# Performance work log

Hardware: AMD Instinct MI355X
Metric: run time of the kernel (lower is better)

Reference implementation:

```python
import jax, jax.numpy as jnp
import numpy as np
from jax.scipy.linalg import cho_solve

N, D, T, K, P = 4000, 256, 52, 20, 100
EPS = 1e-8


def _make_kernel(length_scale):
    # RBF kernel over time grid with the same jitter-doubling rule as the torch code.
    t = np.arange(T, dtype=np.float32)
    sq = (t[None, :] - t[:, None]) ** 2
    Kmat = np.exp(-0.5 * sq / np.float32(length_scale) ** 2).astype(np.float32)
    jitter = 1e-4
    eye = np.eye(T, dtype=np.float32)
    while True:
        if np.linalg.cond(Kmat + jitter * eye) < 1e4:
            break
        jitter *= 2
        if jitter > 0.1:
            break
    return jnp.asarray(Kmat + jitter * eye)

K_LAMBDA = _make_kernel(T / 4)  # lambda GP kernel, shared across all k
K_PHI = _make_kernel(T / 3)     # phi GP kernel, shared across all k


def setup_inputs() -> dict:
    key = jax.random.key(0)
    ks = jax.random.split(key, 7)
    lambda_ = jax.random.normal(ks[0], (N, K, T), dtype=jnp.float32)
    phi = jax.random.normal(ks[1], (K, D, T), dtype=jnp.float32)
    gamma = 0.1 * jax.random.normal(ks[2], (P, K), dtype=jnp.float32)
    G = jax.random.normal(ks[3], (N, P), dtype=jnp.float32)
    Y = (jax.random.uniform(ks[4], (N, D, T)) < 0.05).astype(jnp.float32)
    logit_prev_t = jax.random.normal(ks[5], (D, T), dtype=jnp.float32) - 3.0
    event_times = jax.random.randint(ks[6], (N, D), 0, T)
    return dict(lambda_=lambda_, phi=phi, gamma=gamma, G=G, Y=Y,
                logit_prev_t=logit_prev_t, event_times=event_times)


def reference(lambda_, phi, gamma, G, Y, logit_prev_t, event_times):
    # --- forward: softmax over topics, sigmoid disease probs, mixture ---
    theta = jax.nn.softmax(lambda_, axis=1)          # [N,K,T]
    phi_prob = jax.nn.sigmoid(phi)                   # [K,D,T]
    pi = jnp.einsum('nkt,kdt->ndt', theta, phi_prob) # [N,D,T]
    pi = jnp.clip(pi, EPS, 1.0 - EPS)

    # --- survival data loss ---
    tgrid = jnp.arange(T)[None, None, :]             # [1,1,T]
    e = event_times[:, :, None]                      # [N,D,1]
    mask_before = (tgrid < e).astype(pi.dtype)
    mask_at = (tgrid == e).astype(pi.dtype)
    log_pi = jnp.log(pi)
    log_1mpi = jnp.log1p(-pi)
    loss_censored = -jnp.sum(log_1mpi * mask_before)
    loss_event = -jnp.sum(log_pi * mask_at * Y)
    loss_no_event = -jnp.sum(log_1mpi * mask_at * (1.0 - Y))
    data_loss = (loss_censored + loss_event + loss_no_event) / N

    # --- GP prior loss: batched cholesky solves replace per-sample loops ---
    L_lam = jnp.linalg.cholesky(K_LAMBDA)            # [T,T]
    L_phi = jnp.linalg.cholesky(K_PHI)               # [T,T]
    mean_lam = G @ gamma                             # [N,K]
    dev_lam = (lambda_ - mean_lam[:, :, None]).reshape(N * K, T)  # [N*K,T]
    v_lam = cho_solve((L_lam, True), dev_lam.T)      # [T,N*K]
    gp_lambda = 0.5 * jnp.sum(dev_lam.T * v_lam)
    dev_phi = (phi - logit_prev_t[None, :, :]).reshape(K * D, T)  # [K*D,T]
    v_phi = cho_solve((L_phi, True), dev_phi.T)      # [T,K*D]
    gp_phi = 0.5 * jnp.sum(dev_phi.T * v_phi)
    gp_loss = gp_lambda / N + gp_phi / D

    return data_loss + gp_loss
```

## Files before the change

kernel.cpp:

```cpp
#include <hip/hip_runtime.h>
#include <math.h>
#include <string.h>

#define Nn 4000
#define Dd 256
#define Tt 52
#define Kk 20
#define Pp 100
#define CH 4
#define TC 13
#define GRID_D ((Nn / 8) * CH)

#define OFF_W       0
#define OFF_MLAM_P  5408
#define OFF_MPHI_P  343408
#define OFF_DLP     397488
#define OFF_EVP     399488
#define OFF_PHIP    655488
#define OFF_THETA   921728

#define GR_ROWS 128

#define RB_PHIP0   0
#define RB_THETA0  52
#define RB_GPHI0   865
#define RB_GLAM0   885
#define RB_EVY0    1010
#define RB_TOTAL   2010

__global__ __launch_bounds__(256) void prep_kernel(
    const float* __restrict__ lam, const float* __restrict__ phi,
    const float* __restrict__ gamma, const float* __restrict__ G,
    const float* __restrict__ logit_prev, const int* __restrict__ ev,
    const float* __restrict__ Y,
    float* __restrict__ theta_t, float* __restrict__ phip_t,
    unsigned int* __restrict__ evy,
    float* __restrict__ Mlam_p, float* __restrict__ Mphi_p) {
    __shared__ float rows[GR_ROWS][56];
    __shared__ float meanv[GR_ROWS];
    const int bx = blockIdx.x, tid = threadIdx.x;

    if (bx < RB_THETA0) {
        int gid = bx * 256 + tid;
        int d = gid / Tt, t = gid - d * Tt;
        float v[Kk];
#pragma unroll
        for (int k = 0; k < Kk; ++k) {
            float x = phi[k * (Dd * Tt) + gid];
            v[k] = 1.f / (1.f + __expf(-x));
        }
#pragma unroll
        for (int k = 0; k < Kk; ++k)
            phip_t[((size_t)t * Kk + k) * Dd + d] = v[k];
        return;
    }
    if (bx < RB_GPHI0) {
        int gid = (bx - RB_THETA0) * 256 + tid;
        if (gid >= Nn * Tt) return;
        int n = gid / Tt, t = gid - n * Tt;
        const float* base = lam + n * Kk * Tt + t;
        float v[Kk];
        float m = -1e30f;
#pragma unroll
        for (int k = 0; k < Kk; ++k) { v[k] = base[k * Tt]; m = fmaxf(m, v[k]); }
        float s = 0.f;
#pragma unroll
        for (int k = 0; k < Kk; ++k) { v[k] = __expf(v[k] - m); s += v[k]; }
        float inv = 1.f / s;
        float* o = theta_t + ((size_t)t * Nn + n) * Kk;
#pragma unroll
        for (int k = 0; k < Kk; ++k) o[k] = v[k] * inv;
        return;
    }
    if (bx < RB_GLAM0) {
        int slot = bx - RB_GPHI0;
        int ta = tid % 13, tb = tid / 13;
        float acc[4][4] = {};
        for (int it = 0; it < 2; ++it) {
            int R0 = (slot * 2 + it) * GR_ROWS;
            __syncthreads();
            for (int idx = tid; idx < GR_ROWS * Tt; idx += 256) {
                int r = idx / Tt, t = idx - r * Tt;
                int R = R0 + r;
                rows[r][t] = phi[R * Tt + t] - logit_prev[(R & 255) * Tt + t];
            }
            __syncthreads();
            if (tb < 13) {
                for (int r = 0; r < GR_ROWS; ++r) {
                    float4 a = *(const float4*)&rows[r][4 * ta];
                    float4 b = *(const float4*)&rows[r][4 * tb];
                    float av[4] = {a.x, a.y, a.z, a.w};
                    float bv[4] = {b.x, b.y, b.z, b.w};
#pragma unroll
                    for (int i = 0; i < 4; ++i)
#pragma unroll
                        for (int j = 0; j < 4; ++j) acc[i][j] += av[i] * bv[j];
                }
            }
        }
        if (tb < 13)
#pragma unroll
            for (int i = 0; i < 4; ++i)
#pragma unroll
                for (int j = 0; j < 4; ++j)
                    Mphi_p[slot * 2704 + (4 * ta + i) * Tt + 4 * tb + j] = acc[i][j];
        return;
    }
    if (bx < RB_EVY0) {
        int slot = bx - RB_GLAM0;
        int ta = tid % 13, tb = tid / 13;
        float acc[4][4] = {};
        for (int it = 0; it < 5; ++it) {
            int R0 = (slot * 5 + it) * GR_ROWS;
            __syncthreads();
            if (tid < GR_ROWS) {
                int R = R0 + tid;
                int n = R / Kk, k = R - n * Kk;
                float m = 0.f;
                for (int p = 0; p < Pp; ++p) m += G[n * Pp + p] * gamma[p * Kk + k];
                meanv[tid] = m;
            }
            __syncthreads();
            for (int idx = tid; idx < GR_ROWS * Tt; idx += 256) {
                int r = idx / Tt, t = idx - r * Tt;
                int R = R0 + r;
                rows[r][t] = lam[R * Tt + t] - meanv[r];
            }
            __syncthreads();
            if (tb < 13) {
                for (int r = 0; r < GR_ROWS; ++r) {
                    float4 a = *(const float4*)&rows[r][4 * ta];
                    float4 b = *(const float4*)&rows[r][4 * tb];
                    float av[4] = {a.x, a.y, a.z, a.w};
                    float bv[4] = {b.x, b.y, b.z, b.w};
#pragma unroll
                    for (int i = 0; i < 4; ++i)
#pragma unroll
                        for (int j = 0; j < 4; ++j) acc[i][j] += av[i] * bv[j];
                }
            }
        }
        if (tb < 13)
#pragma unroll
            for (int i = 0; i < 4; ++i)
#pragma unroll
                for (int j = 0; j < 4; ++j)
                    Mlam_p[slot * 2704 + (4 * ta + i) * Tt + 4 * tb + j] = acc[i][j];
        return;
    }
    {
        int idx = bx - RB_EVY0;
        int ng = idx >> 1, half = idx & 1;
        int n0 = ng * 8 + half * 4;
        unsigned a = 0;
#pragma unroll
        for (int g = 0; g < 4; ++g) {
            int nd = (n0 + g) * Dd + tid;
            unsigned e = (unsigned)ev[nd] & 63u;
            float y = __builtin_nontemporal_load(Y + (size_t)nd * Tt + e);
            a |= (e | (y > 0.5f ? 128u : 0u)) << (8 * g);
        }
        evy[((size_t)ng * Dd + tid) * 2 + half] = a;
        return;
    }
}

__global__ __launch_bounds__(256) void data_kernel(const float* __restrict__ theta_t,
                                                   const float* __restrict__ phip_t,
                                                   const uint2* __restrict__ evy,
                                                   float* __restrict__ DLp) {
    __shared__ float wsum[4];
    const int tid = threadIdx.x;
    const int d = tid;
    const int ng = blockIdx.x >> 2;
    const int t0 = (blockIdx.x & 3) * TC;
    const int n0 = ng * 8;

    uint2 ee = evy[(size_t)ng * Dd + d];
    int e[8];
    float Yv[8], acc[8], pie[8], prod[8];
#pragma unroll
    for (int g = 0; g < 8; ++g) {
        unsigned byte = ((g < 4 ? ee.x : ee.y) >> (8 * (g & 3))) & 255u;
        e[g] = (int)(byte & 63u);
        Yv[g] = (byte & 128u) ? 1.f : 0.f;
        acc[g] = 0.f; prod[g] = 1.f; pie[g] = 0.5f;
    }

    for (int j = 0; j < TC; ++j) {
        int t = t0 + j;
        float pv[Kk];
        const float* pt = phip_t + (size_t)t * (Kk * Dd) + d;
#pragma unroll
        for (int k = 0; k < Kk; ++k) pv[k] = pt[k * Dd];
#pragma unroll
        for (int g = 0; g < 8; ++g) {
            const float4* th = (const float4*)(theta_t + ((size_t)t * Nn + n0 + g) * Kk);
            float4 a0 = th[0], a1 = th[1], a2 = th[2], a3 = th[3], a4 = th[4];
            float pi = a0.x * pv[0] + a0.y * pv[1] + a0.z * pv[2] + a0.w * pv[3]
                     + a1.x * pv[4] + a1.y * pv[5] + a1.z * pv[6] + a1.w * pv[7]
                     + a2.x * pv[8] + a2.y * pv[9] + a2.z * pv[10] + a2.w * pv[11]
                     + a3.x * pv[12] + a3.y * pv[13] + a3.z * pv[14] + a3.w * pv[15]
                     + a4.x * pv[16] + a4.y * pv[17] + a4.z * pv[18] + a4.w * pv[19];
            pi = fminf(fmaxf(pi, 1e-8f), 1.0f - 1e-8f);
            prod[g] *= (t <= e[g]) ? (1.f - pi) : 1.f;
            pie[g] = (t == e[g]) ? pi : pie[g];
        }
        if ((j & 3) == 3 || j == TC - 1) {
#pragma unroll
            for (int g = 0; g < 8; ++g) { acc[g] += __logf(prod[g]); prod[g] = 1.f; }
        }
    }
    float tsum = 0.f;
#pragma unroll
    for (int g = 0; g < 8; ++g)
        tsum += acc[g] + Yv[g] * (__logf(pie[g]) - __logf(1.f - pie[g]));
    for (int off = 32; off; off >>= 1) tsum += __shfl_down(tsum, off, 64);
    if ((tid & 63) == 0) wsum[tid >> 6] = tsum;
    __syncthreads();
    if (tid == 0)
        DLp[blockIdx.x] = -(wsum[0] + wsum[1] + wsum[2] + wsum[3]);
}

__global__ __launch_bounds__(1024) void final_kernel(const float* __restrict__ ws,
                                                     float* __restrict__ out) {
    const int tid = threadIdx.x;
    double s = 0.0;
    for (int i = tid; i < 2704; i += 1024) {
        double ml = 0.0, mp = 0.0;
        for (int b = 0; b < 125; ++b) ml += (double)ws[OFF_MLAM_P + b * 2704 + i];
        for (int b = 0; b < 20; ++b)  mp += (double)ws[OFF_MPHI_P + b * 2704 + i];
        s += (double)ws[OFF_W + i] * ml + (double)ws[OFF_W + 2704 + i] * mp;
    }
    double dl = 0.0;
    for (int i = tid; i < GRID_D; i += 1024) dl += (double)ws[OFF_DLP + i];
    s += dl / Nn;
    __shared__ double red[1024];
    red[tid] = s;
    __syncthreads();
    for (int off = 512; off; off >>= 1) {
        if (tid < off) red[tid] += red[tid + off];
        __syncthreads();
    }
    if (tid == 0) out[0] = (float)red[0];
}


static void build_K_f(double ls_in, float Kf[52][52]) {
    float ls = (float)ls_in;
    float ls2 = ls * ls;
    for (int i = 0; i < 52; ++i)
        for (int j = 0; j < 52; ++j) {
            float sq = (float)((i - j) * (i - j));
            float arg = (-0.5f * sq) / ls2;
            Kf[i][j] = expf(arg);
        }
}

static void jacobi_eig(double a[52][52], double ev[52]) {
    const int n = 52;
    for (int sweep = 0; sweep < 100; ++sweep) {
        double off = 0;
        for (int p = 0; p < n - 1; ++p)
            for (int q = p + 1; q < n; ++q) off += a[p][q] * a[p][q];
        if (off < 1e-24) break;
        for (int p = 0; p < n - 1; ++p)
            for (int q = p + 1; q < n; ++q) {
                double apq = a[p][q];
                if (fabs(apq) < 1e-300) continue;
                double th = (a[q][q] - a[p][p]) / (2.0 * apq);
                double t = (th >= 0 ? 1.0 : -1.0) / (fabs(th) + sqrt(th * th + 1.0));
                double c = 1.0 / sqrt(t * t + 1.0), s = t * c;
                for (int i = 0; i < n; ++i) {
                    double aip = a[i][p], aiq = a[i][q];
                    a[i][p] = c * aip - s * aiq;
                    a[i][q] = s * aip + c * aiq;
                }
                for (int i = 0; i < n; ++i) {
                    double api = a[p][i], aqi = a[q][i];
                    a[p][i] = c * api - s * aqi;
                    a[q][i] = s * api + c * aqi;
                }
            }
    }
    for (int i = 0; i < n; ++i) ev[i] = a[i][i];
}

static void build_A(const float Kf[52][52], double jitter, double A[52][52]) {
    float jf = (float)jitter;
    for (int i = 0; i < 52; ++i)
        for (int j = 0; j < 52; ++j) A[i][j] = (double)Kf[i][j];
    for (int i = 0; i < 52; ++i) A[i][i] = (double)(float)(Kf[i][i] + jf);
}

static double cond_of(const float Kf[52][52], double jitter) {
    double A[52][52], ev[52];
    build_A(Kf, jitter, A);
    jacobi_eig(A, ev);
    double mx = 0.0, mn = 1e300;
    for (int i = 0; i < 52; ++i) {
        double a = fabs(ev[i]);
        if (a > mx) mx = a;
        if (a < mn) mn = a;
    }
    if (mn <= 0.0) return 1e300;
    return mx / mn;
}

static double find_jitter(const float Kf[52][52]) {
    double jitter = 1e-4;
    while (true) {
        if (cond_of(Kf, jitter) < 1e4) break;
        jitter *= 2.0;
        if (jitter > 0.1) break;
    }
    return jitter;
}

static void chol_inv_scaled(const float Kf[52][52], double jitter, double scale,
                            float* out) {
    const int n = 52;
    double A[52][52], L[52][52];
    build_A(Kf, jitter, A);
    memset(L, 0, sizeof(L));
    for (int j = 0; j < n; ++j) {
        double s = A[j][j];
        for (int k = 0; k < j; ++k) s -= L[j][k] * L[j][k];
        L[j][j] = sqrt(s);
        for (int i = j + 1; i < n; ++i) {
            double v = A[i][j];
            for (int k = 0; k < j; ++k) v -= L[i][k] * L[j][k];
            L[i][j] = v / L[j][j];
        }
    }
    for (int c = 0; c < n; ++c) {
        double y[52], x[52];
        for (int i = 0; i < n; ++i) {
            double v = (i == c) ? 1.0 : 0.0;
            for (int k = 0; k < i; ++k) v -= L[i][k] * y[k];
            y[i] = v / L[i][i];
        }
        for (int i = n - 1; i >= 0; --i) {
            double v = y[i];
            for (int k = i + 1; k < n; ++k) v -= L[k][i] * x[k];
            x[i] = v / L[i][i];
        }
        for (int i = 0; i < n; ++i) out[i * 52 + c] = (float)(x[i] * scale);
    }
}

struct KinvInit {
    float* w;
    KinvInit() {
        if (hipHostMalloc((void**)&w, 5408 * sizeof(float)) != hipSuccess)
            w = (float*)malloc(5408 * sizeof(float));
        float Kf[52][52];
        build_K_f(52.0 / 4.0, Kf);
        chol_inv_scaled(Kf, find_jitter(Kf), 0.5 / Nn, w);
        build_K_f(52.0 / 3.0, Kf);
        chol_inv_scaled(Kf, find_jitter(Kf), 0.5 / Dd, w + 2704);
    }
};
static KinvInit g_kinv;


extern "C" void kernel_launch(void* const* d_in, const int* in_sizes, int n_in,
                              void* d_out, int out_size, void* d_ws, size_t ws_size,
                              hipStream_t stream) {
    (void)in_sizes; (void)n_in; (void)out_size; (void)ws_size;
    const float* lam        = (const float*)d_in[0];
    const float* phi        = (const float*)d_in[1];
    const float* gamma      = (const float*)d_in[2];
    const float* G          = (const float*)d_in[3];
    const float* Y          = (const float*)d_in[4];
    const float* logit_prev = (const float*)d_in[5];
    const int*   ev         = (const int*)d_in[6];
    float* out = (float*)d_out;
    float* ws  = (float*)d_ws;

    hipMemcpyAsync(ws + OFF_W, g_kinv.w, 5408 * sizeof(float),
                   hipMemcpyHostToDevice, stream);

    prep_kernel<<<RB_TOTAL, 256, 0, stream>>>(
        lam, phi, gamma, G, logit_prev, ev, Y,
        ws + OFF_THETA, ws + OFF_PHIP, (unsigned int*)(ws + OFF_EVP),
        ws + OFF_MLAM_P, ws + OFF_MPHI_P);
    data_kernel<<<GRID_D, 256, 0, stream>>>(
        ws + OFF_THETA, ws + OFF_PHIP, (const uint2*)(ws + OFF_EVP),
        ws + OFF_DLP);
    final_kernel<<<1, 1024, 0, stream>>>(ws, out);
}
```

Baseline: 442.8 us.

## Fuse final reduction into data kernel and reduce Gram partials in-block

The Gram-matrix blocks in the prep kernel now dot their partial 52x52 accumulators with the inverse-kernel weights and block-reduce to a single scalar, replacing the large partial-matrix writes. The final kernel is removed: the last data_kernel block, detected through an atomic counter, sums the partial scalars and data-loss partials. The data kernel also stages the theta tile into shared memory once per block rather than each thread reading it from global memory. This saves a launch and the slow single-block final reduction, at the cost of extra syncs and a threadfence/atomic handshake.

```diff
diff --git a/kernel.cpp b/kernel.cpp
--- a/kernel.cpp
+++ b/kernel.cpp
@@ -12,12 +12,12 @@
 #define GRID_D ((Nn / 8) * CH)
 
 #define OFF_W       0
-#define OFF_MLAM_P  5408
-#define OFF_MPHI_P  343408
-#define OFF_DLP     397488
-#define OFF_EVP     399488
-#define OFF_PHIP    655488
-#define OFF_THETA   921728
+#define OFF_GPART   5408
+#define OFF_DLP     5556
+#define OFF_CNT     7556
+#define OFF_EVP     7560
+#define OFF_PHIP    263560
+#define OFF_THETA   529800
 
 #define GR_ROWS 128
 
@@ -35,12 +35,15 @@
     const float* __restrict__ Y,
     float* __restrict__ theta_t, float* __restrict__ phip_t,
     unsigned int* __restrict__ evy,
-    float* __restrict__ Mlam_p, float* __restrict__ Mphi_p) {
+    const float* __restrict__ W, float* __restrict__ gpart,
+    unsigned int* __restrict__ cnt) {
     __shared__ float rows[GR_ROWS][56];
     __shared__ float meanv[GR_ROWS];
+    __shared__ double redd[256];
     const int bx = blockIdx.x, tid = threadIdx.x;
 
     if (bx < RB_THETA0) {
+        if (bx == 0 && tid == 0) *cnt = 0u;
         int gid = bx * 256 + tid;
         int d = gid / Tt, t = gid - d * Tt;
         float v[Kk];
@@ -98,12 +101,21 @@
                 }
             }
         }
+        double s = 0.0;
         if (tb < 13)
 #pragma unroll
             for (int i = 0; i < 4; ++i)
 #pragma unroll
                 for (int j = 0; j < 4; ++j)
-                    Mphi_p[slot * 2704 + (4 * ta + i) * Tt + 4 * tb + j] = acc[i][j];
+                    s += (double)acc[i][j] *
+                         (double)W[2704 + (4 * ta + i) * Tt + 4 * tb + j];
+        redd[tid] = s;
+        __syncthreads();
+        for (int off = 128; off; off >>= 1) {
+            if (tid < off) redd[tid] += redd[tid + off];
+            __syncthreads();
+        }
+        if (tid == 0) gpart[125 + slot] = (float)redd[0];
         return;
     }
     if (bx < RB_EVY0) {
@@ -140,12 +152,21 @@
                 }
             }
         }
+        double s = 0.0;
         if (tb < 13)
 #pragma unroll
             for (int i = 0; i < 4; ++i)
 #pragma unroll
                 for (int j = 0; j < 4; ++j)
-                    Mlam_p[slot * 2704 + (4 * ta + i) * Tt + 4 * tb + j] = acc[i][j];
+                    s += (double)acc[i][j] *
+                         (double)W[(4 * ta + i) * Tt + 4 * tb + j];
+        redd[tid] = s;
+        __syncthreads();
+        for (int off = 128; off; off >>= 1) {
+            if (tid < off) redd[tid] += redd[tid + off];
+            __syncthreads();
+        }
+        if (tid == 0) gpart[slot] = (float)redd[0];
         return;
     }
     {
@@ -168,14 +189,25 @@
 __global__ __launch_bounds__(256) void data_kernel(const float* __restrict__ theta_t,
                                                    const float* __restrict__ phip_t,
                                                    const uint2* __restrict__ evy,
-                                                   float* __restrict__ DLp) {
+                                                   float* __restrict__ ws,
+                                                   float* __restrict__ out,
+                                                   unsigned int* __restrict__ cnt) {
+    __shared__ __align__(16) float thS[TC][8][Kk];
     __shared__ float wsum[4];
+    __shared__ double redd[256];
+    __shared__ int isLast;
     const int tid = threadIdx.x;
     const int d = tid;
     const int ng = blockIdx.x >> 2;
     const int t0 = (blockIdx.x & 3) * TC;
     const int n0 = ng * 8;
 
+    for (int idx = tid; idx < TC * 160; idx += 256) {
+        int j = idx / 160, r = idx - j * 160;
+        thS[j][r / Kk][r - (r / Kk) * Kk] =
+            theta_t[((size_t)(t0 + j) * Nn + n0) * Kk + r];
+    }
+
     uint2 ee = evy[(size_t)ng * Dd + d];
     int e[8];
     float Yv[8], acc[8], pie[8], prod[8];
@@ -186,6 +218,7 @@
         Yv[g] = (byte & 128u) ? 1.f : 0.f;
         acc[g] = 0.f; prod[g] = 1.f; pie[g] = 0.5f;
     }
+    __syncthreads();
 
     for (int j = 0; j < TC; ++j) {
         int t = t0 + j;
@@ -195,7 +228,7 @@
         for (int k = 0; k < Kk; ++k) pv[k] = pt[k * Dd];
 #pragma unroll
         for (int g = 0; g < 8; ++g) {
-            const float4* th = (const float4*)(theta_t + ((size_t)t * Nn + n0 + g) * Kk);
+            const float4* th = (const float4*)&thS[j][g][0];
             float4 a0 = th[0], a1 = th[1], a2 = th[2], a3 = th[3], a4 = th[4];
             float pi = a0.x * pv[0] + a0.y * pv[1] + a0.z * pv[2] + a0.w * pv[3]
                      + a1.x * pv[4] + a1.y * pv[5] + a1.z * pv[6] + a1.w * pv[7]
@@ -218,31 +251,28 @@
     for (int off = 32; off; off >>= 1) tsum += __shfl_down(tsum, off, 64);
     if ((tid & 63) == 0) wsum[tid >> 6] = tsum;
     __syncthreads();
-    if (tid == 0)
-        DLp[blockIdx.x] = -(wsum[0] + wsum[1] + wsum[2] + wsum[3]);
-}
-
-__global__ __launch_bounds__(1024) void final_kernel(const float* __restrict__ ws,
-                                                     float* __restrict__ out) {
-    const int tid = threadIdx.x;
+    if (tid == 0) {
+        ws[OFF_DLP + blockIdx.x] = -(wsum[0] + wsum[1] + wsum[2] + wsum[3]);
+        __threadfence();
+        unsigned prev = atomicAdd(cnt, 1u);
+        isLast = (prev == GRID_D - 1) ? 1 : 0;
+    }
+    __syncthreads();
+    if (!isLast) return;
+
+    __threadfence();
     double s = 0.0;
-    for (int i = tid; i < 2704; i += 1024) {
-        double ml = 0.0, mp = 0.0;
-        for (int b = 0; b < 125; ++b) ml += (double)ws[OFF_MLAM_P + b * 2704 + i];
-        for (int b = 0; b < 20; ++b)  mp += (double)ws[OFF_MPHI_P + b * 2704 + i];
-        s += (double)ws[OFF_W + i] * ml + (double)ws[OFF_W + 2704 + i] * mp;
-    }
+    for (int i = tid; i < 145; i += 256) s += (double)ws[OFF_GPART + i];
     double dl = 0.0;
-    for (int i = tid; i < GRID_D; i += 1024) dl += (double)ws[OFF_DLP + i];
+    for (int i = tid; i < GRID_D; i += 256) dl += (double)ws[OFF_DLP + i];
     s += dl / Nn;
-    __shared__ double red[1024];
-    red[tid] = s;
+    redd[tid] = s;
     __syncthreads();
-    for (int off = 512; off; off >>= 1) {
-        if (tid < off) red[tid] += red[tid + off];
+    for (int off = 128; off; off >>= 1) {
+        if (tid < off) redd[tid] += redd[tid + off];
         __syncthreads();
     }
-    if (tid == 0) out[0] = (float)red[0];
+    if (tid == 0) out[0] = (float)redd[0];
 }
 
 
@@ -384,9 +414,8 @@
     prep_kernel<<<RB_TOTAL, 256, 0, stream>>>(
         lam, phi, gamma, G, logit_prev, ev, Y,
         ws + OFF_THETA, ws + OFF_PHIP, (unsigned int*)(ws + OFF_EVP),
-        ws + OFF_MLAM_P, ws + OFF_MPHI_P);
+        ws + OFF_W, ws + OFF_GPART, (unsigned int*)(ws + OFF_CNT));
     data_kernel<<<GRID_D, 256, 0, stream>>>(
         ws + OFF_THETA, ws + OFF_PHIP, (const uint2*)(ws + OFF_EVP),
-        ws + OFF_DLP);
-    final_kernel<<<1, 1024, 0, stream>>>(ws, out);
-}
+        ws, out, (unsigned int*)(ws + OFF_CNT));
+}
```

Measured after the change: 435.0 us. About the same (-1.8%).
